# Kernel tuning notes

Hardware: AMD Instinct MI355X
Metric: run time of the kernel (lower is better)

## Reference

```python
import jax, jax.numpy as jnp
import numpy as np

N_DOCS, DOC_LEN, H = 10000, 200, 128   # document token vectors [N, d, h]
B, QLEN, NPIDS = 16, 32, 500           # batch, query tokens, candidate pids per query
TOPK = 100


def setup_inputs() -> dict:
    key = jax.random.key(0)
    k1, k2, k3 = jax.random.split(key, 3)
    q_vectors = jax.random.normal(k1, (B, QLEN, H), dtype=jnp.float32)
    vectors = jax.random.normal(k2, (N_DOCS, DOC_LEN, H), dtype=jnp.float32)
    pids = jax.random.randint(k3, (B, NPIDS), 0, N_DOCS, dtype=jnp.int32)
    boundaries = jnp.array([0, N_DOCS], dtype=jnp.int32)
    return {"q_vectors": q_vectors, "pids": pids, "vectors": vectors,
            "boundaries": boundaries, "k": TOPK}


def _dedupe_row(row):
    # torch.unique-like: sort ascending, replace duplicate entries with -1.
    # (Original pads each row's unique set with -1; only tie-order in the
    #  downstream top-k can differ, the score/pid sets are identical.)
    s = jnp.sort(row)
    dup = jnp.concatenate([jnp.zeros((1,), dtype=bool), s[1:] == s[:-1]])
    return jnp.where(dup, jnp.int32(-1), s)


def reference(q_vectors, pids, vectors, boundaries, k):
    lo = boundaries[0]
    n_vec = vectors.shape[0]
    pids = pids - lo
    pids = jnp.where((pids < 0) | (pids >= n_vec), jnp.int32(-1), pids)
    pids = jax.vmap(_dedupe_row)(pids)                       # [b, K]

    # gather doc token vectors (pid == -1 wraps to last doc; masked below,
    # matching torch's vectors[pids] semantics for -1)
    d_vectors = vectors[pids]                                # [b, K, d, h]
    scores = jnp.einsum('bqh,bkdh->bkqd', q_vectors, d_vectors)
    scores = scores.max(axis=-1).sum(axis=-1)                # MaxSim: max over doc tokens, sum over query tokens -> [b, K]
    scores = jnp.where(pids < 0, -jnp.inf, scores)

    top_scores, top_idx = jax.lax.top_k(scores, k)           # sorted descending
    top_pids = jnp.take_along_axis(pids, top_idx, axis=-1)
    top_pids = jnp.where(top_pids >= 0, top_pids + lo, top_pids)
    return top_scores, top_pids
```

## Files before the change

### kernel.cpp

```cpp
#include <hip/hip_runtime.h>
#include <float.h>
#include <limits.h>

#define NB     16
#define QLEN   32
#define HDIM   128
#define NPIDS  500
#define NDOCS  10000
#define DLEN   200
#define TOPK   100
#define VROW   (DLEN * HDIM)

#define UNIT_BYTES 8192
#define RING_UNITS 4
#define NUNITS     14

typedef _Float16 f16x8 __attribute__((ext_vector_type(8)));
typedef float    f32x16 __attribute__((ext_vector_type(16)));

__global__ __launch_bounds__(512) void dedupe_kernel(const int* __restrict__ pids,
                                                     const int* __restrict__ boundaries,
                                                     int* __restrict__ dpids) {
    __shared__ int s[512];
    const int b = blockIdx.x;
    const int t = threadIdx.x;
    const int lo = boundaries[0];

    int v = INT_MAX;
    if (t < NPIDS) {
        int p = pids[b * NPIDS + t] - lo;
        if (p < 0 || p >= NDOCS) p = -1;
        v = p;
    }
    s[t] = v;
    __syncthreads();

    for (int k = 2; k <= 512; k <<= 1) {
        for (int j = k >> 1; j > 0; j >>= 1) {
            int ixj = t ^ j;
            if (ixj > t) {
                int a = s[t], c = s[ixj];
                bool up = ((t & k) == 0);
                if ((a > c) == up) { s[t] = c; s[ixj] = a; }
            }
            __syncthreads();
        }
    }

    if (t < NPIDS) {
        int val = s[t];
        int o = val;
        if (val == INT_MAX) o = -1;
        else if (t > 0 && val == s[t - 1]) o = -1;
        dpids[b * NPIDS + t] = o;
    }
}

__device__ __forceinline__ void split2h(float a, _Float16& h, _Float16& m) {
    h = (_Float16)a;
    float r = a - (float)h;
    m = (_Float16)r;
}

__device__ __forceinline__ void split2h_pack8(const float4 c0, const float4 c1,
                                              f16x8& H, f16x8& M) {
    float f[8] = {c0.x, c0.y, c0.z, c0.w, c1.x, c1.y, c1.z, c1.w};
    f16x8 Ht, Mt;
    #pragma unroll
    for (int j = 0; j < 8; ++j) {
        _Float16 hh, mm;
        split2h(f[j], hh, mm);
        Ht[j] = hh; Mt[j] = mm;
    }
    H = Ht; M = Mt;
}

__global__ __launch_bounds__(64) void score_kernel(const float* __restrict__ qv,
                                                   const float* __restrict__ vectors,
                                                   const int* __restrict__ dpids,
                                                   float* __restrict__ scores) {
    const int lane = threadIdx.x;
    const int row  = lane & 31;
    const int half = lane >> 5;
    const int cbase = blockIdx.x * 2;
    const int b     = cbase / NPIDS;

    __shared__ __align__(16) unsigned char ring[RING_UNITS * UNIT_BYTES];

    f16x8 qh[8], qm[8];
    {
        const float* qb = qv + ((size_t)b * QLEN + row) * HDIM + half * 8;
        #pragma unroll
        for (int ks = 0; ks < 8; ++ks) {
            const float4 a0 = *(const float4*)(qb + ks * 16);
            const float4 a1 = *(const float4*)(qb + ks * 16 + 4);
            split2h_pack8(a0, a1, qh[ks], qm[ks]);
        }
    }
    __builtin_amdgcn_sched_barrier(0);

    for (int ci = 0; ci < 2; ++ci) {
        const int c   = cbase + ci;
        const int pid = dpids[c];
        if (pid < 0) {
            if (lane == 0) scores[c] = -__builtin_inff();
            continue;
        }

        const char* vcand = (const char*)(vectors + (size_t)pid * VROW);

        auto stage = [&](int u) {
            const int tile = u >> 1, seg = u & 1;
            const int sbase = (u & 3) * UNIT_BYTES;
            #pragma unroll
            for (int i = 0; i < 8; ++i) {
                const int p  = i * 1024 + lane * 16;
                const int tp = p >> 8;
                int tg = tile * 32 + tp;
                if (tg > DLEN - 1) tg = DLEN - 1;
                const unsigned soff = (unsigned)tg * 512u + (unsigned)seg * 256u
                                    + (unsigned)((p & 255) ^ ((tp & 7) << 4));
                __builtin_amdgcn_global_load_lds(
                    (const __attribute__((address_space(1))) void*)(vcand + soff),
                    (__attribute__((address_space(3))) void*)(&ring[sbase + i * 1024]),
                    16, 0, 0);
            }
        };

        float rmax[16];
        #pragma unroll
        for (int j = 0; j < 16; ++j) rmax[j] = -FLT_MAX;

        f32x16 acc;

        stage(0); stage(1); stage(2); stage(3);

        #pragma unroll
        for (int u = 0; u < NUNITS; ++u) {
            if (u <= 10)      asm volatile("s_waitcnt vmcnt(24)" ::: "memory");
            else if (u == 11) asm volatile("s_waitcnt vmcnt(16)" ::: "memory");
            else if (u == 12) asm volatile("s_waitcnt vmcnt(8)"  ::: "memory");
            else              asm volatile("s_waitcnt vmcnt(0)"  ::: "memory");

            if ((u & 1) == 0) {
                #pragma unroll
                for (int j = 0; j < 16; ++j) acc[j] = 0.0f;
            }

            const int ubase = (u & 3) * UNIT_BYTES;
            const int seg   = u & 1;
            const int swz   = (row & 7) << 4;
            #pragma unroll
            for (int k2 = 0; k2 < 4; ++k2) {
                const int ks   = seg * 4 + k2;
                const int off0 = row * 256 + k2 * 64 + half * 32;
                const float4 c0 = *(const float4*)&ring[ubase + (off0 ^ swz)];
                const float4 c1 = *(const float4*)&ring[ubase + ((off0 + 16) ^ swz)];
                f16x8 vh, vm;
                split2h_pack8(c0, c1, vh, vm);
                acc = __builtin_amdgcn_mfma_f32_32x32x16_f16(qh[ks], vh, acc, 0, 0, 0);
                acc = __builtin_amdgcn_mfma_f32_32x32x16_f16(qh[ks], vm, acc, 0, 0, 0);
                acc = __builtin_amdgcn_mfma_f32_32x32x16_f16(qm[ks], vh, acc, 0, 0, 0);
            }

            if (u & 1) {
                #pragma unroll
                for (int j = 0; j < 16; ++j) rmax[j] = fmaxf(rmax[j], acc[j]);
            }

            __builtin_amdgcn_sched_barrier(0);
            if (u + 4 < NUNITS) stage(u + 4);
        }

        double dsum = 0.0;
        #pragma unroll
        for (int j = 0; j < 16; ++j) {
            float m = rmax[j];
            m = fmaxf(m, __shfl_xor(m, 1));
            m = fmaxf(m, __shfl_xor(m, 2));
            m = fmaxf(m, __shfl_xor(m, 4));
            m = fmaxf(m, __shfl_xor(m, 8));
            m = fmaxf(m, __shfl_xor(m, 16));
            dsum += (double)m;
        }
        dsum += __shfl_xor(dsum, 32);
        if (lane == 0) scores[c] = (float)dsum;
    }
}

__global__ __launch_bounds__(512) void topk_kernel(const float* __restrict__ scores,
                                                   const int* __restrict__ dpids,
                                                   const int* __restrict__ boundaries,
                                                   float* __restrict__ out) {
    __shared__ float ss[512];
    __shared__ int   sp[512];
    const int b = blockIdx.x;
    const int t = threadIdx.x;
    const int lo = boundaries[0];

    float sc = -__builtin_inff();
    int   p  = -1;
    if (t < NPIDS) {
        p = dpids[b * NPIDS + t];
        sc = (p < 0) ? -__builtin_inff() : scores[b * NPIDS + t];
    }
    ss[t] = sc;
    sp[t] = p;
    __syncthreads();

    for (int k = 2; k <= 512; k <<= 1) {
        for (int j = k >> 1; j > 0; j >>= 1) {
            int ixj = t ^ j;
            if (ixj > t) {
                float a = ss[t], c = ss[ixj];
                bool down = ((t & k) == 0);
                bool swap = down ? (a < c) : (a > c);
                if (swap) {
                    int pa = sp[t], pc = sp[ixj];
                    ss[t] = c;   ss[ixj] = a;
                    sp[t] = pc;  sp[ixj] = pa;
                }
            }
            __syncthreads();
        }
    }

    if (t < TOPK) {
        out[b * TOPK + t] = ss[t];
        int pp = sp[t];
        out[NB * TOPK + b * TOPK + t] = (pp >= 0) ? (float)(pp + lo) : -1.0f;
    }
}

extern "C" void kernel_launch(void* const* d_in, const int* in_sizes, int n_in,
                              void* d_out, int out_size, void* d_ws, size_t ws_size,
                              hipStream_t stream) {
    const float* qv        = (const float*)d_in[0];
    const int*   pids      = (const int*)d_in[1];
    const float* vectors   = (const float*)d_in[2];
    const int*   boundaries= (const int*)d_in[3];

    int*   dpids  = (int*)d_ws;
    float* scores = (float*)((char*)d_ws + 32768);

    dedupe_kernel<<<NB, 512, 0, stream>>>(pids, boundaries, dpids);
    score_kernel <<<(NB * NPIDS) / 2, 64, 0, stream>>>(qv, vectors, dpids, scores);
    topk_kernel  <<<NB, 512, 0, stream>>>(scores, dpids, boundaries, (float*)d_out);
}
```

Baseline: 168.0 us.

## Group candidate jobs by pid so one block scores a document for two queries

Adds a histogram/scan/scatter/pair pipeline that buckets all (batch, pid) jobs by document id and pairs jobs sharing the same pid into one entry. Each score block then streams a document's vectors once and runs MFMAs against two query batches, reducing global memory traffic for repeated pids. It adds five small extra kernel launches, atomics, and a serial single-block scan over 10001 bins. Blocks are launched for a fixed 8192 entries and exit early on sentinels. With random pids, duplicates across batches are modest (8000 jobs over 10000 docs), so pairing opportunities are limited.

```diff
diff --git a/kernel.cpp b/kernel.cpp
--- a/kernel.cpp
+++ b/kernel.cpp
@@ -10,6 +10,10 @@
 #define DLEN   200
 #define TOPK   100
 #define VROW   (DLEN * HDIM)
+#define NJOBS  (NB * NPIDS)
+#define NBINS  (NDOCS + 1)
+#define NENT   8192
+#define SENT   0x7FFFFFFF
 
 #define UNIT_BYTES 8192
 #define RING_UNITS 4
@@ -56,6 +60,88 @@
     }
 }
 
+__global__ __launch_bounds__(512) void init_kernel(int* __restrict__ counts,
+                                                   int* __restrict__ counter,
+                                                   int2* __restrict__ entries) {
+    int i = blockIdx.x * 512 + threadIdx.x;
+    if (i < NBINS) counts[i] = 0;
+    if (i == 0) *counter = 0;
+    if (i < NENT) entries[i] = make_int2(SENT, -1);
+}
+
+__global__ __launch_bounds__(512) void hist_kernel(const int* __restrict__ dpids,
+                                                   int* __restrict__ counts) {
+    int i = blockIdx.x * 512 + threadIdx.x;
+    if (i < NJOBS) {
+        int p = dpids[i];
+        int key = (p < 0) ? NDOCS : p;
+        atomicAdd(&counts[key], 1);
+    }
+}
+
+__global__ __launch_bounds__(512) void scan_kernel(const int* __restrict__ counts,
+                                                   int* __restrict__ offsets,
+                                                   int* __restrict__ offsets0) {
+    __shared__ int tmp[512];
+    __shared__ int carry;
+    const int t = threadIdx.x;
+    if (t == 0) carry = 0;
+    __syncthreads();
+
+    for (int base = 0; base < NBINS; base += 512) {
+        int x = (base + t < NBINS) ? counts[base + t] : 0;
+        tmp[t] = x;
+        __syncthreads();
+        for (int off = 1; off < 512; off <<= 1) {
+            int v = (t >= off) ? tmp[t - off] : 0;
+            __syncthreads();
+            tmp[t] += v;
+            __syncthreads();
+        }
+        if (base + t < NBINS) {
+            int e = carry + tmp[t] - x;
+            offsets[base + t]  = e;
+            offsets0[base + t] = e;
+        }
+        int btot = tmp[511];
+        __syncthreads();
+        if (t == 0) carry += btot;
+        __syncthreads();
+    }
+}
+
+__global__ __launch_bounds__(512) void scatter_kernel(const int* __restrict__ dpids,
+                                                      int* __restrict__ offsets,
+                                                      int* __restrict__ jobs) {
+    int i = blockIdx.x * 512 + threadIdx.x;
+    if (i < NJOBS) {
+        int p = dpids[i];
+        int key = (p < 0) ? NDOCS : p;
+        int pos = atomicAdd(&offsets[key], 1);
+        jobs[pos] = (key << 13) | i;
+    }
+}
+
+__global__ __launch_bounds__(512) void pair_kernel(const int* __restrict__ jobs,
+                                                   const int* __restrict__ offsets0,
+                                                   int* __restrict__ counter,
+                                                   int2* __restrict__ entries) {
+    int i = blockIdx.x * 512 + threadIdx.x;
+    if (i >= NJOBS) return;
+    int e   = jobs[i];
+    int key = e >> 13;
+    int ja  = e & 8191;
+    int rs  = offsets0[key];
+    if (((i - rs) & 1) != 0) return;
+    int jb = -1;
+    if (i + 1 < NJOBS) {
+        int e2 = jobs[i + 1];
+        if ((e2 >> 13) == key) jb = e2 & 8191;
+    }
+    int pos = atomicAdd(counter, 1);
+    entries[pos] = make_int2(key, (jb << 16) | ja);
+}
+
 __device__ __forceinline__ void split2h(float a, _Float16& h, _Float16& m) {
     h = (_Float16)a;
     float r = a - (float)h;
@@ -75,107 +161,127 @@
     H = Ht; M = Mt;
 }
 
+__device__ __forceinline__ void load_q_limbs(const float* __restrict__ qv, int b,
+                                             int row, int half, f16x8* qh, f16x8* qm) {
+    const float* qb = qv + ((size_t)b * QLEN + row) * HDIM + half * 8;
+    #pragma unroll
+    for (int ks = 0; ks < 8; ++ks) {
+        const float4 a0 = *(const float4*)(qb + ks * 16);
+        const float4 a1 = *(const float4*)(qb + ks * 16 + 4);
+        split2h_pack8(a0, a1, qh[ks], qm[ks]);
+    }
+}
+
 __global__ __launch_bounds__(64) void score_kernel(const float* __restrict__ qv,
                                                    const float* __restrict__ vectors,
-                                                   const int* __restrict__ dpids,
+                                                   const int2* __restrict__ entries,
                                                    float* __restrict__ scores) {
     const int lane = threadIdx.x;
     const int row  = lane & 31;
     const int half = lane >> 5;
-    const int cbase = blockIdx.x * 2;
-    const int b     = cbase / NPIDS;
+
+    const int bid = blockIdx.x;
+    const int v   = (bid & 7) * (NENT / 8) + (bid >> 3);
+
+    const int2 ent = entries[v];
+    const int pid  = ent.x;
+    if (pid == SENT) return;
+    const int ja = ent.y & 0xFFFF;
+    const int jb = ent.y >> 16;
+    if (pid >= NDOCS) {
+        if (lane == 0) {
+            scores[ja] = -__builtin_inff();
+            if (jb >= 0) scores[jb] = -__builtin_inff();
+        }
+        return;
+    }
+    const bool dual = (jb >= 0);
 
     __shared__ __align__(16) unsigned char ring[RING_UNITS * UNIT_BYTES];
 
-    f16x8 qh[8], qm[8];
+    f16x8 qhA[8], qmA[8], qhB[8], qmB[8];
+    load_q_limbs(qv, ja / NPIDS, row, half, qhA, qmA);
+    if (dual) load_q_limbs(qv, jb / NPIDS, row, half, qhB, qmB);
+    __builtin_amdgcn_sched_barrier(0);
+
+    const char* vcand = (const char*)(vectors + (size_t)pid * VROW);
+
+    auto stage = [&](int u) {
+        const int tile = u >> 1, seg = u & 1;
+        const int sbase = (u & 3) * UNIT_BYTES;
+        #pragma unroll
+        for (int i = 0; i < 8; ++i) {
+            const int p  = i * 1024 + lane * 16;
+            const int tp = p >> 8;
+            int tg = tile * 32 + tp;
+            if (tg > DLEN - 1) tg = DLEN - 1;
+            const unsigned soff = (unsigned)tg * 512u + (unsigned)seg * 256u
+                                + (unsigned)((p & 255) ^ ((tp & 7) << 4));
+            __builtin_amdgcn_global_load_lds(
+                (const __attribute__((address_space(1))) void*)(vcand + soff),
+                (__attribute__((address_space(3))) void*)(&ring[sbase + i * 1024]),
+                16, 0, 0);
+        }
+    };
+
+    float rmaxA[16], rmaxB[16];
+    #pragma unroll
+    for (int j = 0; j < 16; ++j) { rmaxA[j] = -FLT_MAX; rmaxB[j] = -FLT_MAX; }
+
+    f32x16 accA, accB;
+
+    stage(0); stage(1); stage(2); stage(3);
+
+    #pragma unroll
+    for (int u = 0; u < NUNITS; ++u) {
+        if (u <= 10)      asm volatile("s_waitcnt vmcnt(24)" ::: "memory");
+        else if (u == 11) asm volatile("s_waitcnt vmcnt(16)" ::: "memory");
+        else if (u == 12) asm volatile("s_waitcnt vmcnt(8)"  ::: "memory");
+        else              asm volatile("s_waitcnt vmcnt(0)"  ::: "memory");
+
+        if ((u & 1) == 0) {
+            #pragma unroll
+            for (int j = 0; j < 16; ++j) { accA[j] = 0.0f; accB[j] = 0.0f; }
+        }
+
+        const int ubase = (u & 3) * UNIT_BYTES;
+        const int seg   = u & 1;
+        const int swz   = (row & 7) << 4;
+        #pragma unroll
+        for (int k2 = 0; k2 < 4; ++k2) {
+            const int ks   = seg * 4 + k2;
+            const int off0 = row * 256 + k2 * 64 + half * 32;
+            const float4 c0 = *(const float4*)&ring[ubase + (off0 ^ swz)];
+            const float4 c1 = *(const float4*)&ring[ubase + ((off0 + 16) ^ swz)];
+            f16x8 vh, vm;
+            split2h_pack8(c0, c1, vh, vm);
+            accA = __builtin_amdgcn_mfma_f32_32x32x16_f16(qhA[ks], vh, accA, 0, 0, 0);
+            accA = __builtin_amdgcn_mfma_f32_32x32x16_f16(qhA[ks], vm, accA, 0, 0, 0);
+            accA = __builtin_amdgcn_mfma_f32_32x32x16_f16(qmA[ks], vh, accA, 0, 0, 0);
+            if (dual) {
+                accB = __builtin_amdgcn_mfma_f32_32x32x16_f16(qhB[ks], vh, accB, 0, 0, 0);
+                accB = __builtin_amdgcn_mfma_f32_32x32x16_f16(qhB[ks], vm, accB, 0, 0, 0);
+                accB = __builtin_amdgcn_mfma_f32_32x32x16_f16(qmB[ks], vh, accB, 0, 0, 0);
+            }
+        }
+
+        if (u & 1) {
+            #pragma unroll
+            for (int j = 0; j < 16; ++j) {
+                rmaxA[j] = fmaxf(rmaxA[j], accA[j]);
+                rmaxB[j] = fmaxf(rmaxB[j], accB[j]);
+            }
+        }
+
+        __builtin_amdgcn_sched_barrier(0);
+        if (u + 4 < NUNITS) stage(u + 4);
+    }
+
     {
-        const float* qb = qv + ((size_t)b * QLEN + row) * HDIM + half * 8;
-        #pragma unroll
-        for (int ks = 0; ks < 8; ++ks) {
-            const float4 a0 = *(const float4*)(qb + ks * 16);
-            const float4 a1 = *(const float4*)(qb + ks * 16 + 4);
-            split2h_pack8(a0, a1, qh[ks], qm[ks]);
-        }
-    }
-    __builtin_amdgcn_sched_barrier(0);
-
-    for (int ci = 0; ci < 2; ++ci) {
-        const int c   = cbase + ci;
-        const int pid = dpids[c];
-        if (pid < 0) {
-            if (lane == 0) scores[c] = -__builtin_inff();
-            continue;
-        }
-
-        const char* vcand = (const char*)(vectors + (size_t)pid * VROW);
-
-        auto stage = [&](int u) {
-            const int tile = u >> 1, seg = u & 1;
-            const int sbase = (u & 3) * UNIT_BYTES;
-            #pragma unroll
-            for (int i = 0; i < 8; ++i) {
-                const int p  = i * 1024 + lane * 16;
-                const int tp = p >> 8;
-                int tg = tile * 32 + tp;
-                if (tg > DLEN - 1) tg = DLEN - 1;
-                const unsigned soff = (unsigned)tg * 512u + (unsigned)seg * 256u
-                                    + (unsigned)((p & 255) ^ ((tp & 7) << 4));
-                __builtin_amdgcn_global_load_lds(
-                    (const __attribute__((address_space(1))) void*)(vcand + soff),
-                    (__attribute__((address_space(3))) void*)(&ring[sbase + i * 1024]),
-                    16, 0, 0);
-            }
-        };
-
-        float rmax[16];
-        #pragma unroll
-        for (int j = 0; j < 16; ++j) rmax[j] = -FLT_MAX;
-
-        f32x16 acc;
-
-        stage(0); stage(1); stage(2); stage(3);
-
-        #pragma unroll
-        for (int u = 0; u < NUNITS; ++u) {
-            if (u <= 10)      asm volatile("s_waitcnt vmcnt(24)" ::: "memory");
-            else if (u == 11) asm volatile("s_waitcnt vmcnt(16)" ::: "memory");
-            else if (u == 12) asm volatile("s_waitcnt vmcnt(8)"  ::: "memory");
-            else              asm volatile("s_waitcnt vmcnt(0)"  ::: "memory");
-
-            if ((u & 1) == 0) {
-                #pragma unroll
-                for (int j = 0; j < 16; ++j) acc[j] = 0.0f;
-            }
-
-            const int ubase = (u & 3) * UNIT_BYTES;
-            const int seg   = u & 1;
-            const int swz   = (row & 7) << 4;
-            #pragma unroll
-            for (int k2 = 0; k2 < 4; ++k2) {
-                const int ks   = seg * 4 + k2;
-                const int off0 = row * 256 + k2 * 64 + half * 32;
-                const float4 c0 = *(const float4*)&ring[ubase + (off0 ^ swz)];
-                const float4 c1 = *(const float4*)&ring[ubase + ((off0 + 16) ^ swz)];
-                f16x8 vh, vm;
-                split2h_pack8(c0, c1, vh, vm);
-                acc = __builtin_amdgcn_mfma_f32_32x32x16_f16(qh[ks], vh, acc, 0, 0, 0);
-                acc = __builtin_amdgcn_mfma_f32_32x32x16_f16(qh[ks], vm, acc, 0, 0, 0);
-                acc = __builtin_amdgcn_mfma_f32_32x32x16_f16(qm[ks], vh, acc, 0, 0, 0);
-            }
-
-            if (u & 1) {
-                #pragma unroll
-                for (int j = 0; j < 16; ++j) rmax[j] = fmaxf(rmax[j], acc[j]);
-            }
-
-            __builtin_amdgcn_sched_barrier(0);
-            if (u + 4 < NUNITS) stage(u + 4);
-        }
-
         double dsum = 0.0;
         #pragma unroll
         for (int j = 0; j < 16; ++j) {
-            float m = rmax[j];
+            float m = rmaxA[j];
             m = fmaxf(m, __shfl_xor(m, 1));
             m = fmaxf(m, __shfl_xor(m, 2));
             m = fmaxf(m, __shfl_xor(m, 4));
@@ -184,7 +290,22 @@
             dsum += (double)m;
         }
         dsum += __shfl_xor(dsum, 32);
-        if (lane == 0) scores[c] = (float)dsum;
+        if (lane == 0) scores[ja] = (float)dsum;
+    }
+    if (dual) {
+        double dsum = 0.0;
+        #pragma unroll
+        for (int j = 0; j < 16; ++j) {
+            float m = rmaxB[j];
+            m = fmaxf(m, __shfl_xor(m, 1));
+            m = fmaxf(m, __shfl_xor(m, 2));
+            m = fmaxf(m, __shfl_xor(m, 4));
+            m = fmaxf(m, __shfl_xor(m, 8));
+            m = fmaxf(m, __shfl_xor(m, 16));
+            dsum += (double)m;
+        }
+        dsum += __shfl_xor(dsum, 32);
+        if (lane == 0) scores[jb] = (float)dsum;
     }
 }
 
@@ -240,10 +361,22 @@
     const float* vectors   = (const float*)d_in[2];
     const int*   boundaries= (const int*)d_in[3];
 
-    int*   dpids  = (int*)d_ws;
-    float* scores = (float*)((char*)d_ws + 32768);
-
-    dedupe_kernel<<<NB, 512, 0, stream>>>(pids, boundaries, dpids);
-    score_kernel <<<(NB * NPIDS) / 2, 64, 0, stream>>>(qv, vectors, dpids, scores);
-    topk_kernel  <<<NB, 512, 0, stream>>>(scores, dpids, boundaries, (float*)d_out);
-}
+    char* ws = (char*)d_ws;
+    int*   dpids    = (int*)(ws);
+    float* scores   = (float*)(ws + 32768);
+    int*   counts   = (int*)(ws + 65536);
+    int*   offsets  = (int*)(ws + 114688);
+    int*   offsets0 = (int*)(ws + 163840);
+    int*   jobs     = (int*)(ws + 212992);
+    int2*  entries  = (int2*)(ws + 262144);
+    int*   counter  = (int*)(ws + 327680);
+
+    dedupe_kernel <<<NB, 512, 0, stream>>>(pids, boundaries, dpids);
+    init_kernel   <<<(NBINS + 511) / 512, 512, 0, stream>>>(counts, counter, entries);
+    hist_kernel   <<<(NJOBS + 511) / 512, 512, 0, stream>>>(dpids, counts);
+    scan_kernel   <<<1, 512, 0, stream>>>(counts, offsets, offsets0);
+    scatter_kernel<<<(NJOBS + 511) / 512, 512, 0, stream>>>(dpids, offsets, jobs);
+    pair_kernel   <<<(NJOBS + 511) / 512, 512, 0, stream>>>(jobs, offsets0, counter, entries);
+    score_kernel  <<<NENT, 64, 0, stream>>>(qv, vectors, entries, scores);
+    topk_kernel   <<<NB, 512, 0, stream>>>(scores, dpids, boundaries, (float*)d_out);
+}
```

Result: slower. 235.4 us (+40.1%).
